# Optimization experiments

Hardware: AMD Instinct MI355X
Metric: run time of the kernel (lower is better)

The kernel has to match this reference:

```python
import jax, jax.numpy as jnp
import numpy as np

SIGMA = 1.0  # kernel bandwidth (init kwarg)

VS = 4096   # src vertices
VT = 4096   # tar vertices
FS = 8192   # src triangles
FT = 8192   # tar triangles
FR = 8192   # reference triangles


def setup_inputs() -> dict:
    key = jax.random.key(0)
    k0, k1, k2, k3, k4, k5 = jax.random.split(key, 6)
    src_vertices = jax.random.normal(k0, (VS, 3), dtype=jnp.float32)
    src_indices = jax.random.randint(k1, (FS, 3), 0, VS, dtype=jnp.int64)
    tar_vertices = jax.random.normal(k2, (VT, 3), dtype=jnp.float32)
    tar_indices = jax.random.randint(k3, (FT, 3), 0, VT, dtype=jnp.int64)
    ref_normals = 0.1 * jax.random.normal(k4, (FR, 3), dtype=jnp.float32)
    ref_centers = jax.random.normal(k5, (FR, 3), dtype=jnp.float32)
    return {
        "src_vertices": src_vertices,
        "src_indices": src_indices,
        "tar_vertices": tar_vertices,
        "tar_indices": tar_indices,
        "ref_normals": ref_normals,
        "ref_centers": ref_centers,
    }


def _tri_normals_centers(vertices, indices):
    tris = vertices[indices]               # [F, 3, 3]
    a, b, c = tris[:, 0, :], tris[:, 1, :], tris[:, 2, :]
    normals = 0.5 * jnp.cross(a - b, c - b)  # [F, 3]
    centers = tris.sum(axis=1) / 3.0         # [F, 3]
    return normals, centers


def _sqdist(src, tar):
    # d[i, j] = ||tar_i - src_j||^2  -> shape [Nt, Ns]
    s2 = jnp.sum(src * src, axis=-1)  # [Ns]
    t2 = jnp.sum(tar * tar, axis=-1)  # [Nt]
    return t2[:, None] + s2[None, :] - 2.0 * (tar @ src.T)


def _cauchy(d):
    return 1.0 / (1.0 + d / SIGMA) ** 2


def _energy(sn, sc, tn, tc):
    e1 = jnp.sum((sn @ sn.T) * _cauchy(_sqdist(sc, sc)))
    e2 = jnp.sum((tn @ sn.T) * _cauchy(_sqdist(sc, tc)))
    e3 = jnp.sum((tn @ tn.T) * _cauchy(_sqdist(tc, tc)))
    return e1 - 2.0 * e2 + e3


def reference(src_vertices, src_indices, tar_vertices, tar_indices, ref_normals, ref_centers):
    src_n, src_c = _tri_normals_centers(src_vertices, src_indices)
    tar_n, tar_c = _tri_normals_centers(tar_vertices, tar_indices)
    energy = _energy(src_n, src_c, ref_normals, ref_centers)
    energy = energy + _energy(tar_n, tar_c, ref_normals, ref_centers)
    energy = energy + 0.8 * _energy(src_n, src_c, tar_n, tar_c)
    return energy
```

## Files before the change

kernel.cpp:

```cpp
#include <hip/hip_runtime.h>

#define NSEG 8192
#define NPTS (3 * NSEG)
#define NSUP 96
#define NY   49

typedef short bf16x8 __attribute__((ext_vector_type(8)));
typedef float f32x16 __attribute__((ext_vector_type(16)));
typedef unsigned short u16;

__device__ __forceinline__ u16 f2bf(float x) {
    unsigned u = __builtin_bit_cast(unsigned, x);
    return (u16)((u + 0x7FFFu + ((u >> 16) & 1u)) >> 16);
}
__device__ __forceinline__ float bf2f(u16 h) {
    unsigned u = ((unsigned)h) << 16;
    return __builtin_bit_cast(float, u);
}

__device__ __forceinline__ void compute_point(
    int seg, int f,
    const float* __restrict__ sv, const int* __restrict__ si,
    const float* __restrict__ tv, const int* __restrict__ ti,
    const float* __restrict__ rn, const float* __restrict__ rc,
    float& cx, float& cy, float& cz, float& nx, float& ny, float& nz)
{
    if (seg == 2) {
        nx = rn[3*f];   ny = rn[3*f+1]; nz = rn[3*f+2];
        cx = rc[3*f];   cy = rc[3*f+1]; cz = rc[3*f+2];
    } else {
        const float* v  = (seg == 0) ? sv : tv;
        const int*   nd = (seg == 0) ? si : ti;
        int i0 = nd[3*f], i1 = nd[3*f+1], i2 = nd[3*f+2];
        float ax = v[3*i0], ay = v[3*i0+1], az = v[3*i0+2];
        float bx = v[3*i1], by = v[3*i1+1], bz = v[3*i1+2];
        float gx = v[3*i2], gy = v[3*i2+1], gz = v[3*i2+2];
        float ux = ax-bx, uy = ay-by, uz = az-bz;
        float wx = gx-bx, wy = gy-by, wz = gz-bz;
        nx = 0.5f*(uy*wz - uz*wy);
        ny = 0.5f*(uz*wx - ux*wz);
        nz = 0.5f*(ux*wy - uy*wx);
        cx = (ax+bx+gx)*(1.0f/3.0f);
        cy = (ay+by+gy)*(1.0f/3.0f);
        cz = (az+bz+gz)*(1.0f/3.0f);
    }
}

__global__ void setup_feats(const float* __restrict__ sv, const int* __restrict__ si,
                            const float* __restrict__ tv, const int* __restrict__ ti,
                            const float* __restrict__ rn, const float* __restrict__ rc,
                            u16* __restrict__ ws, float* __restrict__ out) {
    int p = blockIdx.x * 256 + threadIdx.x;
    if (p == 0) out[0] = 0.0f;
    if (p >= NPTS) return;
    int seg = p >> 13, f = p & (NSEG - 1);
    float cx, cy, cz, nx, ny, nz;
    compute_point(seg, f, sv, si, tv, ti, rn, rc, cx, cy, cz, nx, ny, nz);

    const u16 ONE = 0x3F80;
    float s = cx*cx + cy*cy + cz*cz;
    u16 chx = f2bf(cx), chy = f2bf(cy), chz = f2bf(cz);
    u16 clx = f2bf(cx - bf2f(chx)), cly = f2bf(cy - bf2f(chy)), clz = f2bf(cz - bf2f(chz));
    u16 sh  = f2bf(s);
    u16 sl  = f2bf(s - bf2f(sh));
    u16 m2hx = f2bf(-2.0f*bf2f(chx)), m2hy = f2bf(-2.0f*bf2f(chy)), m2hz = f2bf(-2.0f*bf2f(chz));
    u16 m2lx = f2bf(-2.0f*bf2f(clx)), m2ly = f2bf(-2.0f*bf2f(cly)), m2lz = f2bf(-2.0f*bf2f(clz));
    u16 nhx = f2bf(nx), nhy = f2bf(ny), nhz = f2bf(nz);
    u16 nlx = f2bf(nx - bf2f(nhx)), nly = f2bf(ny - bf2f(nhy)), nlz = f2bf(nz - bf2f(nhz));

    u16 at[16] = {chx,chy,chz, clx,cly,clz, chx,chy,chz, sh, sl, ONE, ONE, ONE, 0, 0};
    u16 bt[16] = {m2hx,m2hy,m2hz, m2hx,m2hy,m2hz, m2lx,m2ly,m2lz, ONE, ONE, sh, sl, ONE, 0, 0};
    u16 an[16] = {nhx,nhy,nhz, nlx,nly,nlz, nhx,nhy,nhz, 0,0,0,0,0,0,0};
    u16 bn[16] = {nhx,nhy,nhz, nhx,nhy,nhz, nlx,nly,nlz, 0,0,0,0,0,0,0};

    bf16x8* A8 = (bf16x8*)ws;
    bf16x8* B8 = A8 + (size_t)NPTS*4;
    bf16x8 v0, v1, v2, v3;
    #pragma unroll
    for (int k = 0; k < 8; ++k) { v0[k] = (short)at[k]; v1[k] = (short)at[k+8];
                                  v2[k] = (short)an[k]; v3[k] = (short)an[k+8]; }
    A8[(size_t)p*4+0] = v0; A8[(size_t)p*4+1] = v1; A8[(size_t)p*4+2] = v2; A8[(size_t)p*4+3] = v3;
    #pragma unroll
    for (int k = 0; k < 8; ++k) { v0[k] = (short)bt[k]; v1[k] = (short)bt[k+8];
                                  v2[k] = (short)bn[k]; v3[k] = (short)bn[k+8]; }
    B8[(size_t)p*4+0] = v0; B8[(size_t)p*4+1] = v1; B8[(size_t)p*4+2] = v2; B8[(size_t)p*4+3] = v3;
}

__launch_bounds__(256, 3)
__global__ void energy_mfma(const u16* __restrict__ ws, float* __restrict__ out) {
    const int tid  = threadIdx.x;
    const int lane = tid & 63, wid = tid >> 6;
    const int half = lane >> 5, r32 = lane & 31;

    const int X = blockIdx.x;
    const int Y = blockIdx.y;
    int J = X + Y; if (J >= NSUP) J -= NSUP;
    const int gi = X >> 5;
    const int gj = J >> 5;

    const float Wt[9] = {1.8f, -0.8f, -1.0f,
                        -0.8f,  1.8f, -1.0f,
                        -1.0f, -1.0f,  2.0f};
    const float mult = (Y == 0 || Y == 48) ? 1.0f : 2.0f;
    const float w = Wt[gi*3 + gj] * mult;

    const bf16x8* A8 = (const bf16x8*)ws;
    const bf16x8* B8 = A8 + (size_t)NPTS*4;

    const int pi0 = X*256 + wid*64 + r32;
    const bf16x8 at0 = A8[pi0*4 + half];
    const bf16x8 an0 = A8[pi0*4 + 2 + half];
    const bf16x8 at1 = A8[(pi0+32)*4 + half];
    const bf16x8 an1 = A8[(pi0+32)*4 + 2 + half];

    f32x16 Z;
    #pragma unroll
    for (int k = 0; k < 16; ++k) Z[k] = 0.0f;

    const int base = J*1024 + r32*4 + half;

    bf16x8 btf = B8[base];
    bf16x8 bnf = B8[base + 2];

    float ts0 = 0.0f, ts1 = 0.0f;
    #pragma unroll 2
    for (int jt = 0; jt < 8; ++jt) {
        int nofs = base + ((jt < 7) ? (jt + 1) : jt) * 128;
        bf16x8 nbt = B8[nofs];
        bf16x8 nbn = B8[nofs + 2];

        f32x16 ct0 = __builtin_amdgcn_mfma_f32_32x32x16_bf16(at0, btf, Z, 0, 0, 0);
        f32x16 cn0 = __builtin_amdgcn_mfma_f32_32x32x16_bf16(an0, bnf, Z, 0, 0, 0);
        f32x16 ct1 = __builtin_amdgcn_mfma_f32_32x32x16_bf16(at1, btf, Z, 0, 0, 0);
        f32x16 cn1 = __builtin_amdgcn_mfma_f32_32x32x16_bf16(an1, bnf, Z, 0, 0, 0);

        #pragma unroll
        for (int g = 0; g < 4; ++g) {
            {
                float t0 = ct0[4*g+0], t1 = ct0[4*g+1], t2 = ct0[4*g+2], t3 = ct0[4*g+3];
                float q0 = t0*t0, q1 = t1*t1, q2 = t2*t2, q3 = t3*t3;
                float s01 = q0*q1, s23 = q2*q3;
                float r   = __builtin_amdgcn_rcpf(s01*s23);
                float u   = __builtin_fmaf(cn0[4*g+1], q0, cn0[4*g+0]*q1);
                float v   = __builtin_fmaf(cn0[4*g+3], q2, cn0[4*g+2]*q3);
                float num = __builtin_fmaf(v, s01, u*s23);
                ts0 = __builtin_fmaf(num, r, ts0);
            }
            {
                float t0 = ct1[4*g+0], t1 = ct1[4*g+1], t2 = ct1[4*g+2], t3 = ct1[4*g+3];
                float q0 = t0*t0, q1 = t1*t1, q2 = t2*t2, q3 = t3*t3;
                float s01 = q0*q1, s23 = q2*q3;
                float r   = __builtin_amdgcn_rcpf(s01*s23);
                float u   = __builtin_fmaf(cn1[4*g+1], q0, cn1[4*g+0]*q1);
                float v   = __builtin_fmaf(cn1[4*g+3], q2, cn1[4*g+2]*q3);
                float num = __builtin_fmaf(v, s01, u*s23);
                ts1 = __builtin_fmaf(num, r, ts1);
            }
        }

        btf = nbt; bnf = nbn;
    }
    float acc = w * (ts0 + ts1);

    for (int off = 32; off; off >>= 1) acc += __shfl_down(acc, off, 64);
    __shared__ float partial[4];
    if ((tid & 63) == 0) partial[wid] = acc;
    __syncthreads();
    if (tid == 0)
        atomicAdd(out, (partial[0] + partial[1]) + (partial[2] + partial[3]));
}

extern "C" void kernel_launch(void* const* d_in, const int* in_sizes, int n_in,
                              void* d_out, int out_size, void* d_ws, size_t ws_size,
                              hipStream_t stream) {
    const float* sv = (const float*)d_in[0];
    const int*   si = (const int*)d_in[1];
    const float* tv = (const float*)d_in[2];
    const int*   ti = (const int*)d_in[3];
    const float* rn = (const float*)d_in[4];
    const float* rc = (const float*)d_in[5];
    float* out = (float*)d_out;
    u16*   ws  = (u16*)d_ws;

    setup_feats<<<NPTS/256, 256, 0, stream>>>(sv, si, tv, ti, rn, rc, ws, out);
    dim3 grid(NSUP, NY);
    energy_mfma<<<grid, 256, 0, stream>>>(ws, out);
}
```

Measured before the change: 134.7 us.

## Switch pair-energy kernel to 16x16x32 MFMA tiles with multi-diagonal blocks

Replaces the 32x32x16 bf16 MFMA tiles with 16x16x32 tiles. The K=16 feature vectors are padded by zeroing the upper half-wave's operands. Supertiles shrink to 128 rows, and each block loops over four diagonal offsets with double-buffered B loads. Launch bounds rise to 6 blocks per CU. The aim is fewer accumulator registers, higher occupancy and less per-block launch overhead, at the cost of doing twice the MFMA work per output, since half of each K=32 reduction is zeros.

```diff
diff --git a/kernel.cpp b/kernel.cpp
--- a/kernel.cpp
+++ b/kernel.cpp
@@ -2,11 +2,11 @@
 
 #define NSEG 8192
 #define NPTS (3 * NSEG)
-#define NSUP 96
-#define NY   49
+#define NSUP 192
+#define NYG  25
 
 typedef short bf16x8 __attribute__((ext_vector_type(8)));
-typedef float f32x16 __attribute__((ext_vector_type(16)));
+typedef float f32x4  __attribute__((ext_vector_type(4)));
 typedef unsigned short u16;
 
 __device__ __forceinline__ u16 f2bf(float x) {
@@ -86,81 +86,87 @@
     B8[(size_t)p*4+0] = v0; B8[(size_t)p*4+1] = v1; B8[(size_t)p*4+2] = v2; B8[(size_t)p*4+3] = v3;
 }
 
-__launch_bounds__(256, 3)
+__launch_bounds__(256, 6)
 __global__ void energy_mfma(const u16* __restrict__ ws, float* __restrict__ out) {
     const int tid  = threadIdx.x;
     const int lane = tid & 63, wid = tid >> 6;
-    const int half = lane >> 5, r32 = lane & 31;
+    const int n16  = lane & 15, q = (lane >> 4) & 1;
+    const bool lo  = lane < 32;
 
     const int X = blockIdx.x;
-    const int Y = blockIdx.y;
-    int J = X + Y; if (J >= NSUP) J -= NSUP;
-    const int gi = X >> 5;
-    const int gj = J >> 5;
+    const int g = blockIdx.y;
+    const int y0 = 4*g;
+    const int cnt = (g == 24) ? 1 : 4;
+    const int gi = X >> 6;
 
     const float Wt[9] = {1.8f, -0.8f, -1.0f,
                         -0.8f,  1.8f, -1.0f,
                         -1.0f, -1.0f,  2.0f};
-    const float mult = (Y == 0 || Y == 48) ? 1.0f : 2.0f;
-    const float w = Wt[gi*3 + gj] * mult;
 
     const bf16x8* A8 = (const bf16x8*)ws;
     const bf16x8* B8 = A8 + (size_t)NPTS*4;
 
-    const int pi0 = X*256 + wid*64 + r32;
-    const bf16x8 at0 = A8[pi0*4 + half];
-    const bf16x8 an0 = A8[pi0*4 + 2 + half];
-    const bf16x8 at1 = A8[(pi0+32)*4 + half];
-    const bf16x8 an1 = A8[(pi0+32)*4 + 2 + half];
+    bf16x8 at0, an0, at1, an1;
+    #pragma unroll
+    for (int k = 0; k < 8; ++k) { at0[k] = 0; an0[k] = 0; at1[k] = 0; an1[k] = 0; }
+    const int pi = X*128 + wid*32 + n16;
+    if (lo) {
+        at0 = A8[pi*4 + q];        an0 = A8[pi*4 + 2 + q];
+        at1 = A8[(pi+16)*4 + q];   an1 = A8[(pi+16)*4 + 2 + q];
+    }
 
-    f32x16 Z;
+    f32x4 Z = {0.0f, 0.0f, 0.0f, 0.0f};
+
+    bf16x8 bT[2], bN[2];
     #pragma unroll
-    for (int k = 0; k < 16; ++k) Z[k] = 0.0f;
+    for (int k = 0; k < 8; ++k) { bT[0][k] = 0; bT[1][k] = 0; bN[0][k] = 0; bN[1][k] = 0; }
 
-    const int base = J*1024 + r32*4 + half;
+    float acc = 0.0f;
+    for (int yy = 0; yy < cnt; ++yy) {
+        const int y = y0 + yy;
+        int J = X + y; if (J >= NSUP) J -= NSUP;
+        const float mult = (y == 0 || y == 96) ? 1.0f : 2.0f;
+        const float w = Wt[gi*3 + (J >> 6)] * mult;
 
-    bf16x8 btf = B8[base];
-    bf16x8 bnf = B8[base + 2];
+        const int bbase = (J*128 + n16)*4 + q;
+        if (lo) { bT[0] = B8[bbase]; bN[0] = B8[bbase + 2]; }
 
-    float ts0 = 0.0f, ts1 = 0.0f;
-    #pragma unroll 2
-    for (int jt = 0; jt < 8; ++jt) {
-        int nofs = base + ((jt < 7) ? (jt + 1) : jt) * 128;
-        bf16x8 nbt = B8[nofs];
-        bf16x8 nbn = B8[nofs + 2];
+        float ts0 = 0.0f, ts1 = 0.0f;
+        #pragma unroll
+        for (int jt = 0; jt < 8; ++jt) {
+            const int cur = jt & 1, nxt = cur ^ 1;
+            if (jt < 7 && lo) {
+                bT[nxt] = B8[bbase + (jt+1)*64];
+                bN[nxt] = B8[bbase + (jt+1)*64 + 2];
+            }
+            f32x4 ct0 = __builtin_amdgcn_mfma_f32_16x16x32_bf16(at0, bT[cur], Z, 0, 0, 0);
+            f32x4 cn0 = __builtin_amdgcn_mfma_f32_16x16x32_bf16(an0, bN[cur], Z, 0, 0, 0);
+            f32x4 ct1 = __builtin_amdgcn_mfma_f32_16x16x32_bf16(at1, bT[cur], Z, 0, 0, 0);
+            f32x4 cn1 = __builtin_amdgcn_mfma_f32_16x16x32_bf16(an1, bN[cur], Z, 0, 0, 0);
 
-        f32x16 ct0 = __builtin_amdgcn_mfma_f32_32x32x16_bf16(at0, btf, Z, 0, 0, 0);
-        f32x16 cn0 = __builtin_amdgcn_mfma_f32_32x32x16_bf16(an0, bnf, Z, 0, 0, 0);
-        f32x16 ct1 = __builtin_amdgcn_mfma_f32_32x32x16_bf16(at1, btf, Z, 0, 0, 0);
-        f32x16 cn1 = __builtin_amdgcn_mfma_f32_32x32x16_bf16(an1, bnf, Z, 0, 0, 0);
-
-        #pragma unroll
-        for (int g = 0; g < 4; ++g) {
             {
-                float t0 = ct0[4*g+0], t1 = ct0[4*g+1], t2 = ct0[4*g+2], t3 = ct0[4*g+3];
-                float q0 = t0*t0, q1 = t1*t1, q2 = t2*t2, q3 = t3*t3;
+                float q0 = ct0[0]*ct0[0], q1 = ct0[1]*ct0[1];
+                float q2 = ct0[2]*ct0[2], q3 = ct0[3]*ct0[3];
                 float s01 = q0*q1, s23 = q2*q3;
                 float r   = __builtin_amdgcn_rcpf(s01*s23);
-                float u   = __builtin_fmaf(cn0[4*g+1], q0, cn0[4*g+0]*q1);
-                float v   = __builtin_fmaf(cn0[4*g+3], q2, cn0[4*g+2]*q3);
+                float u   = __builtin_fmaf(cn0[1], q0, cn0[0]*q1);
+                float v   = __builtin_fmaf(cn0[3], q2, cn0[2]*q3);
                 float num = __builtin_fmaf(v, s01, u*s23);
                 ts0 = __builtin_fmaf(num, r, ts0);
             }
             {
-                float t0 = ct1[4*g+0], t1 = ct1[4*g+1], t2 = ct1[4*g+2], t3 = ct1[4*g+3];
-                float q0 = t0*t0, q1 = t1*t1, q2 = t2*t2, q3 = t3*t3;
+                float q0 = ct1[0]*ct1[0], q1 = ct1[1]*ct1[1];
+                float q2 = ct1[2]*ct1[2], q3 = ct1[3]*ct1[3];
                 float s01 = q0*q1, s23 = q2*q3;
                 float r   = __builtin_amdgcn_rcpf(s01*s23);
-                float u   = __builtin_fmaf(cn1[4*g+1], q0, cn1[4*g+0]*q1);
-                float v   = __builtin_fmaf(cn1[4*g+3], q2, cn1[4*g+2]*q3);
+                float u   = __builtin_fmaf(cn1[1], q0, cn1[0]*q1);
+                float v   = __builtin_fmaf(cn1[3], q2, cn1[2]*q3);
                 float num = __builtin_fmaf(v, s01, u*s23);
                 ts1 = __builtin_fmaf(num, r, ts1);
             }
         }
-
-        btf = nbt; bnf = nbn;
+        acc = __builtin_fmaf(w, ts0 + ts1, acc);
     }
-    float acc = w * (ts0 + ts1);
 
     for (int off = 32; off; off >>= 1) acc += __shfl_down(acc, off, 64);
     __shared__ float partial[4];
@@ -183,6 +189,6 @@
     u16*   ws  = (u16*)d_ws;
 
     setup_feats<<<NPTS/256, 256, 0, stream>>>(sv, si, tv, ti, rn, rc, ws, out);
-    dim3 grid(NSUP, NY);
+    dim3 grid(NSUP, NYG);
     energy_mfma<<<grid, 256, 0, stream>>>(ws, out);
 }
```

Result: slower. 450.1 us (+234.3%).
